# Optimization experiments

Hardware: AMD Instinct MI355X
Metric: run time of the kernel (lower is better)

Reference implementation:

```python
import jax, jax.numpy as jnp
import numpy as np

N, E = 50000, 800000
IN_DIM, HID, HEADS, LAYERS = 128, 128, 4, 2
C = HID // HEADS  # per-head channels
LN_EPS = 1e-5


def _segment_softmax(logits, seg, num_segments):
    # logits: [E, H], seg: [E] target-node ids
    m = jax.ops.segment_max(logits, seg, num_segments=num_segments)  # [N, H]
    ex = jnp.exp(logits - m[seg])
    s = jax.ops.segment_sum(ex, seg, num_segments=num_segments)      # [N, H]
    return ex / s[seg]


def setup_inputs() -> dict:
    key = jax.random.key(0)
    ks = jax.random.split(key, 16)
    x = jax.random.normal(ks[0], (N, IN_DIM), dtype=jnp.float32)
    edge_index = jax.random.randint(ks[1], (2, E), 0, N, dtype=jnp.int64)
    edge_weight = jax.random.normal(ks[2], (E,), dtype=jnp.float32)
    s = 0.05
    # stacked per-layer params (in_ch == hidden for both layers since in_dim == hidden_dim)
    Wq = jax.random.normal(ks[3], (LAYERS, HID, HID), dtype=jnp.float32) * s
    bq = jnp.zeros((LAYERS, HID), dtype=jnp.float32)
    Wk = jax.random.normal(ks[4], (LAYERS, HID, HID), dtype=jnp.float32) * s
    bk = jnp.zeros((LAYERS, HID), dtype=jnp.float32)
    Wv = jax.random.normal(ks[5], (LAYERS, HID, HID), dtype=jnp.float32) * s
    bv = jnp.zeros((LAYERS, HID), dtype=jnp.float32)
    We = jax.random.normal(ks[6], (LAYERS, 1, HID), dtype=jnp.float32) * s  # lin_edge, no bias
    Wskip = jax.random.normal(ks[7], (LAYERS, HID, HID), dtype=jnp.float32) * s
    bskip = jnp.zeros((LAYERS, HID), dtype=jnp.float32)
    ln_g = jnp.ones((LAYERS, HID), dtype=jnp.float32)
    ln_b = jnp.zeros((LAYERS, HID), dtype=jnp.float32)
    return dict(x=x, edge_index=edge_index, edge_weight=edge_weight,
                Wq=Wq, bq=bq, Wk=Wk, bk=bk, Wv=Wv, bv=bv, We=We,
                Wskip=Wskip, bskip=bskip, ln_g=ln_g, ln_b=ln_b)


def reference(x, edge_index, edge_weight, Wq, bq, Wk, bk, Wv, bv, We, Wskip, bskip, ln_g, ln_b):
    # eval mode: dropout (on alpha and on features) is identity
    h = jnp.nan_to_num(x, nan=0.0, posinf=0.0, neginf=0.0)
    edge_attr = jnp.nan_to_num(edge_weight, nan=0.0, posinf=0.0, neginf=0.0)[:, None]  # [E,1]
    src, dst = edge_index[0], edge_index[1]  # PyG: x_j = x[src], softmax/aggregate over dst
    scale = 1.0 / jnp.sqrt(jnp.asarray(C, dtype=h.dtype))
    for l in range(LAYERS):
        h_res = h
        q = (h @ Wq[l] + bq[l]).reshape(N, HEADS, C)
        k = (h @ Wk[l] + bk[l]).reshape(N, HEADS, C)
        v = (h @ Wv[l] + bv[l]).reshape(N, HEADS, C)
        e = (edge_attr @ We[l]).reshape(E, HEADS, C)          # lin_edge (bias=False)
        kj = k[src] + e                                       # [E,H,C]
        logits = jnp.einsum('ehc,ehc->eh', q[dst], kj) * scale
        alpha = _segment_softmax(logits, dst, N)              # [E,H]
        msg = (v[src] + e) * alpha[..., None]                 # [E,H,C]
        out = jax.ops.segment_sum(msg, dst, num_segments=N).reshape(N, HID)
        out = out + h @ Wskip[l] + bskip[l]                   # root_weight skip (beta=False)
        out = jnp.nan_to_num(out, nan=0.0, posinf=0.0, neginf=0.0)
        mu = out.mean(axis=-1, keepdims=True)
        var = ((out - mu) ** 2).mean(axis=-1, keepdims=True)
        out = (out - mu) / jnp.sqrt(var + LN_EPS) * ln_g[l] + ln_b[l]
        out = jax.nn.relu(jnp.nan_to_num(out, nan=0.0, posinf=0.0, neginf=0.0))
        out = jnp.nan_to_num(out, nan=0.0, posinf=0.0, neginf=0.0)
        h = jnp.nan_to_num(out + h_res, nan=0.0, posinf=0.0, neginf=0.0)
    return h
```

## Files before the change

kernel.cpp:

```cpp
#include <hip/hip_runtime.h>
#include <hip/hip_fp16.h>
#include <math.h>

#define NN 50000
#define EE 800000
#define HID 128
#define LAYERS 2
#define LN_EPS 1e-5f
#define SCALE 0.17677669529663687f

typedef _Float16 f16x8 __attribute__((ext_vector_type(8)));
typedef float f32x4 __attribute__((ext_vector_type(4)));

__device__ __forceinline__ float sanitize(float f) {
    return (f == f && fabsf(f) != INFINITY) ? f : 0.0f;
}


__global__ void zero_deg_kernel(int* __restrict__ deg) {
    int i = blockIdx.x * blockDim.x + threadIdx.x;
    if (i < NN) deg[i] = 0;
}

__global__ void hist_kernel(const int* __restrict__ eidx, int* __restrict__ deg) {
    int e = blockIdx.x * blockDim.x + threadIdx.x;
    if (e < EE) atomicAdd(&deg[eidx[EE + e]], 1);
}

__global__ __launch_bounds__(1024) void scan_kernel(const int* __restrict__ deg,
                                                    int* __restrict__ row_start,
                                                    int* __restrict__ cursor) {
    __shared__ int wsum[16];
    __shared__ int carry_s;
    int tid = threadIdx.x;
    int lane = tid & 63;
    int wid = tid >> 6;
    if (tid == 0) carry_s = 0;
    __syncthreads();
    for (int base = 0; base < NN; base += 1024) {
        int i = base + tid;
        int val = (i < NN) ? deg[i] : 0;
        int sc = val;
        #pragma unroll
        for (int off = 1; off < 64; off <<= 1) {
            int t = __shfl_up(sc, off, 64);
            if (lane >= off) sc += t;
        }
        if (lane == 63) wsum[wid] = sc;
        __syncthreads();
        if (wid == 0) {
            int s = (lane < 16) ? wsum[lane] : 0;
            #pragma unroll
            for (int off = 1; off < 16; off <<= 1) {
                int t = __shfl_up(s, off, 64);
                if (lane >= off) s += t;
            }
            if (lane < 16) wsum[lane] = s;
        }
        __syncthreads();
        int waveoff = (wid > 0) ? wsum[wid - 1] : 0;
        int excl = carry_s + waveoff + sc - val;
        if (i < NN) {
            row_start[i] = excl;
            cursor[i] = excl;
        }
        __syncthreads();
        if (tid == 0) carry_s += wsum[15];
        __syncthreads();
    }
    if (tid == 0) row_start[NN] = carry_s;
}

__global__ void scatter_kernel(const int* __restrict__ eidx,
                               const float* __restrict__ ew,
                               int* __restrict__ cursor,
                               long long* __restrict__ csr_pk) {
    int e = blockIdx.x * blockDim.x + threadIdx.x;
    if (e < EE) {
        int dst = eidx[EE + e];
        int src = eidx[e];
        int pos = atomicAdd(&cursor[dst], 1);
        unsigned wb = __float_as_uint(sanitize(ew[e]));
        csr_pk[pos] = ((long long)wb << 32) | (unsigned)src;
    }
}


__global__ void sanitize_kernel(const float* __restrict__ x, float* __restrict__ h0,
                                __half* __restrict__ hh) {
    int i = blockIdx.x * blockDim.x + threadIdx.x;
    if (i < NN * HID / 4) {
        float4 f = ((const float4*)x)[i];
        f.x = sanitize(f.x); f.y = sanitize(f.y); f.z = sanitize(f.z); f.w = sanitize(f.w);
        ((float4*)h0)[i] = f;
        __half2* hp = (__half2*)(hh + (size_t)i * 4);
        hp[0] = __floats2half2_rn(f.x, f.y);
        hp[1] = __floats2half2_rn(f.z, f.w);
    }
}


__global__ void wtcvt_kernel(const float* __restrict__ Wq, const float* __restrict__ Wk,
                             const float* __restrict__ Wv, __half* __restrict__ WT) {
    int idx = blockIdx.x * blockDim.x + threadIdx.x;
    if (idx >= LAYERS * 3 * HID * HID) return;
    int k = idx & 127;
    int c = (idx >> 7) & 127;
    int lm = idx >> 14;
    int m = lm % 3;
    int l = lm / 3;
    const float* W = (m == 0) ? Wq : (m == 1) ? Wk : Wv;
    WT[idx] = __float2half(W[l * HID * HID + k * HID + c]);
}


__global__ __launch_bounds__(256) void mfma_qkv_kernel(
    const __half* __restrict__ hh, const __half* __restrict__ WT,
    const float* __restrict__ bq, const float* __restrict__ bk, const float* __restrict__ bv,
    __half* __restrict__ qh, __half* __restrict__ kv)
{
    int wid = threadIdx.x >> 6;
    int lane = threadIdx.x & 63;
    int row0 = blockIdx.x * 64 + wid * 16;
    int arow = row0 + (lane & 15);
    if (arow >= NN) arow = NN - 1;
    int ksub = (lane >> 4) * 8;

    const _Float16* hp = (const _Float16*)(hh + (size_t)arow * HID + ksub);
    f16x8 a0 = *(const f16x8*)(hp + 0);
    f16x8 a1 = *(const f16x8*)(hp + 32);
    f16x8 a2 = *(const f16x8*)(hp + 64);
    f16x8 a3 = *(const f16x8*)(hp + 96);

    #pragma unroll
    for (int m = 0; m < 3; ++m) {
        const _Float16* Wm = (const _Float16*)(WT + m * HID * HID);
        const float* bias = (m == 0) ? bq : (m == 1) ? bk : bv;
        #pragma unroll
        for (int t = 0; t < 8; ++t) {
            int col = t * 16 + (lane & 15);
            const _Float16* wc = Wm + (size_t)col * HID + ksub;
            f32x4 acc = {0.f, 0.f, 0.f, 0.f};
            acc = __builtin_amdgcn_mfma_f32_16x16x32_f16(a0, *(const f16x8*)(wc + 0),  acc, 0, 0, 0);
            acc = __builtin_amdgcn_mfma_f32_16x16x32_f16(a1, *(const f16x8*)(wc + 32), acc, 0, 0, 0);
            acc = __builtin_amdgcn_mfma_f32_16x16x32_f16(a2, *(const f16x8*)(wc + 64), acc, 0, 0, 0);
            acc = __builtin_amdgcn_mfma_f32_16x16x32_f16(a3, *(const f16x8*)(wc + 96), acc, 0, 0, 0);
            float bcol = bias[col];
            #pragma unroll
            for (int r = 0; r < 4; ++r) {
                int row = row0 + (lane >> 4) * 4 + r;
                if (row < NN) {
                    __half val = __float2half(acc[r] + bcol);
                    if (m == 0)      qh[(size_t)row * HID + col] = val;
                    else if (m == 1) kv[(size_t)row * 256 + col] = val;
                    else             kv[(size_t)row * 256 + 128 + col] = val;
                }
            }
        }
    }
}


#define GR 64
#define GK 32

__global__ __launch_bounds__(256) void gemm_skip_kernel(
    const float* __restrict__ hin, const float* __restrict__ W,
    const float* __restrict__ b, float* __restrict__ o)
{
    __shared__ float sh[GR][GK];
    __shared__ float sw[GK][HID];

    const int tid = threadIdx.x;
    const int cg = tid & 31;
    const int rg = tid >> 5;
    const int row0 = blockIdx.x * GR;

    float4 acc[8];
    #pragma unroll
    for (int r = 0; r < 8; ++r) acc[r] = make_float4(0.f, 0.f, 0.f, 0.f);

    for (int kc = 0; kc < HID; kc += GK) {
        __syncthreads();
        #pragma unroll
        for (int p = 0; p < 2; ++p) {
            int idx = p * 256 + tid;
            int r = idx >> 3;
            int c4 = idx & 7;
            int grow = row0 + r;
            float4 hv = make_float4(0.f, 0.f, 0.f, 0.f);
            if (grow < NN) hv = *(const float4*)(hin + (size_t)grow * HID + kc + c4 * 4);
            *(float4*)(&sh[r][c4 * 4]) = hv;
        }
        #pragma unroll
        for (int p = 0; p < 4; ++p) {
            int idx = p * 256 + tid;
            ((float4*)sw)[idx] = ((const float4*)(W + (size_t)kc * HID))[idx];
        }
        __syncthreads();

        #pragma unroll
        for (int k4 = 0; k4 < GK; k4 += 4) {
            float4 b0 = *(float4*)(&sw[k4 + 0][cg * 4]);
            float4 b1 = *(float4*)(&sw[k4 + 1][cg * 4]);
            float4 b2 = *(float4*)(&sw[k4 + 2][cg * 4]);
            float4 b3 = *(float4*)(&sw[k4 + 3][cg * 4]);
            #pragma unroll
            for (int rr = 0; rr < 8; ++rr) {
                float4 a = *(float4*)(&sh[rg * 8 + rr][k4]);
                float4 t = acc[rr];
                t.x = fmaf(a.x, b0.x, fmaf(a.y, b1.x, fmaf(a.z, b2.x, fmaf(a.w, b3.x, t.x))));
                t.y = fmaf(a.x, b0.y, fmaf(a.y, b1.y, fmaf(a.z, b2.y, fmaf(a.w, b3.y, t.y))));
                t.z = fmaf(a.x, b0.z, fmaf(a.y, b1.z, fmaf(a.z, b2.z, fmaf(a.w, b3.z, t.z))));
                t.w = fmaf(a.x, b0.w, fmaf(a.y, b1.w, fmaf(a.z, b2.w, fmaf(a.w, b3.w, t.w))));
                acc[rr] = t;
            }
        }
    }

    float4 bias = *(const float4*)(b + cg * 4);
    #pragma unroll
    for (int rr = 0; rr < 8; ++rr) {
        int grow = row0 + rg * 8 + rr;
        if (grow < NN) {
            float4 t = acc[rr];
            t.x += bias.x; t.y += bias.y; t.z += bias.z; t.w += bias.w;
            *(float4*)(o + (size_t)grow * HID + cg * 4) = t;
        }
    }
}


__device__ __forceinline__ float red16(float x) {
    #pragma unroll
    for (int off = 8; off >= 1; off >>= 1) x += __shfl_xor(x, off, 16);
    return x;
}

__device__ __forceinline__ float red64(float x) {
    #pragma unroll
    for (int off = 32; off >= 1; off >>= 1) x += __shfl_xor(x, off, 64);
    return x;
}

struct OS { float m, s, tw, ax, ay; };

__device__ __forceinline__ void os_init(OS& o) {
    o.m = -INFINITY; o.s = 0.f; o.tw = 0.f; o.ax = 0.f; o.ay = 0.f;
}

__device__ __forceinline__ void os_upd(OS& o, float l, float w, float vx, float vy) {
    float mn = fmaxf(o.m, l);
    float cr = __expf(o.m - mn);
    float p  = __expf(l - mn);
    o.s  = fmaf(o.s,  cr, p);
    o.tw = fmaf(o.tw, cr, p * w);
    o.ax = fmaf(o.ax, cr, p * vx);
    o.ay = fmaf(o.ay, cr, p * vy);
    o.m = mn;
}

__device__ __forceinline__ OS os_mrg(OS a, OS b) {
    float mn = fmaxf(a.m, b.m);
    if (mn == -INFINITY) return a;
    float ca = __expf(a.m - mn);
    float cb = __expf(b.m - mn);
    OS r;
    r.m = mn;
    r.s  = a.s  * ca + b.s  * cb;
    r.tw = a.tw * ca + b.tw * cb;
    r.ax = a.ax * ca + b.ax * cb;
    r.ay = a.ay * ca + b.ay * cb;
    return r;
}

__device__ __forceinline__ void edge_step(const long long* __restrict__ csr_pk, int i,
                                          const __half* __restrict__ kv, int lane,
                                          float qx, float qy, float qwe, OS& st) {
    long long p = csr_pk[i];
    int src = (int)(p & 0xffffffffLL);
    float w = __uint_as_float((unsigned)((unsigned long long)p >> 32));
    const __half* kvp = kv + (size_t)src * 256;
    float2 k2 = __half22float2(*(const __half2*)(kvp + 2 * lane));
    float2 v2 = __half22float2(*(const __half2*)(kvp + 128 + 2 * lane));
    float d = red16(fmaf(k2.x, qx, k2.y * qy));
    float l = fmaf(w, qwe, d) * SCALE;
    os_upd(st, l, w, v2.x, v2.y);
}

__global__ __launch_bounds__(256) void agg_kernel(
    const __half* __restrict__ qh, const __half* __restrict__ kv,
    const float* __restrict__ skp, const float* __restrict__ hres,
    const float* __restrict__ We,
    const float* __restrict__ ln_g, const float* __restrict__ ln_b,
    const int* __restrict__ row_start, const long long* __restrict__ csr_pk,
    float* __restrict__ hout, __half* __restrict__ hh_out)
{
    int node = blockIdx.x * 4 + (threadIdx.x >> 6);
    if (node >= NN) return;
    int lane = threadIdx.x & 63;
    int c0 = lane * 2;

    float2 q2 = __half22float2(*(const __half2*)(qh + (size_t)node * HID + c0));
    float2 we2 = *(const float2*)(We + c0);
    float qwe = red16(fmaf(q2.x, we2.x, q2.y * we2.y));

    int rs = row_start[node];
    int re = row_start[node + 1];

    OS st0, st1, st2, st3;
    os_init(st0); os_init(st1); os_init(st2); os_init(st3);

    int i = rs;
    for (; i + 4 <= re; i += 4) {
        edge_step(csr_pk, i + 0, kv, lane, q2.x, q2.y, qwe, st0);
        edge_step(csr_pk, i + 1, kv, lane, q2.x, q2.y, qwe, st1);
        edge_step(csr_pk, i + 2, kv, lane, q2.x, q2.y, qwe, st2);
        edge_step(csr_pk, i + 3, kv, lane, q2.x, q2.y, qwe, st3);
    }
    for (; i < re; ++i) edge_step(csr_pk, i, kv, lane, q2.x, q2.y, qwe, st0);

    OS st = os_mrg(os_mrg(st0, st1), os_mrg(st2, st3));

    float ox = 0.f, oy = 0.f;
    if (re > rs) {
        float inv = 1.f / st.s;
        ox = fmaf(st.tw, we2.x, st.ax) * inv;
        oy = fmaf(st.tw, we2.y, st.ay) * inv;
    }

    float2 sk = *(const float2*)(skp + (size_t)node * HID + c0);
    ox = sanitize(ox + sk.x);
    oy = sanitize(oy + sk.y);

    float mu = red64(ox + oy) * (1.f / 128.f);
    float dx = ox - mu, dy = oy - mu;
    float var = red64(fmaf(dx, dx, dy * dy)) * (1.f / 128.f);
    float rstd = rsqrtf(var + LN_EPS);

    float2 g = *(const float2*)(ln_g + c0);
    float2 bb = *(const float2*)(ln_b + c0);
    float rx = fmaxf(fmaf(dx * rstd, g.x, bb.x), 0.f);
    float ry = fmaxf(fmaf(dy * rstd, g.y, bb.y), 0.f);

    float2 hr = *(const float2*)(hres + (size_t)node * HID + c0);
    float outx = sanitize(rx + hr.x);
    float outy = sanitize(ry + hr.y);
    *(float2*)(hout + (size_t)node * HID + c0) = make_float2(outx, outy);
    *(__half2*)(hh_out + (size_t)node * HID + c0) = __floats2half2_rn(outx, outy);
}


extern "C" void kernel_launch(void* const* d_in, const int* in_sizes, int n_in,
                              void* d_out, int out_size, void* d_ws, size_t ws_size,
                              hipStream_t stream) {
    const float* x      = (const float*)d_in[0];
    const int*   ei     = (const int*)d_in[1];
    const float* ew     = (const float*)d_in[2];
    const float* Wq     = (const float*)d_in[3];
    const float* bq     = (const float*)d_in[4];
    const float* Wk     = (const float*)d_in[5];
    const float* bk     = (const float*)d_in[6];
    const float* Wv     = (const float*)d_in[7];
    const float* bv     = (const float*)d_in[8];
    const float* We     = (const float*)d_in[9];
    const float* Wsk    = (const float*)d_in[10];
    const float* bsk    = (const float*)d_in[11];
    const float* ln_g   = (const float*)d_in[12];
    const float* ln_b   = (const float*)d_in[13];

    const size_t NH = (size_t)NN * HID;
    float* h0 = (float*)d_ws;
    float* h1 = h0 + NH;
    float* sk = h1 + NH;
    __half* hh = (__half*)(sk + NH);
    __half* qh = hh + NH;
    __half* kv = qh + NH;
    __half* WT = kv + 2 * NH;
    int* deg       = (int*)(WT + LAYERS * 3 * HID * HID);
    int* row_start = deg + NN;
    int* cursor    = row_start + NN + 2;
    long long* csr_pk = (long long*)(cursor + NN);

    zero_deg_kernel<<<(NN + 255) / 256, 256, 0, stream>>>(deg);
    hist_kernel<<<(EE + 255) / 256, 256, 0, stream>>>(ei, deg);
    scan_kernel<<<1, 1024, 0, stream>>>(deg, row_start, cursor);
    scatter_kernel<<<(EE + 255) / 256, 256, 0, stream>>>(ei, ew, cursor, csr_pk);

    sanitize_kernel<<<(NN * HID / 4 + 255) / 256, 256, 0, stream>>>(x, h0, hh);
    wtcvt_kernel<<<(LAYERS * 3 * HID * HID + 255) / 256, 256, 0, stream>>>(Wq, Wk, Wv, WT);

    const int WELEM = HID * HID;
    const int MROWS = (NN + 63) / 64;

    for (int l = 0; l < LAYERS; ++l) {
        const float* hin = (l == 0) ? h0 : h1;
        float* hout = (l == 0) ? h1 : (float*)d_out;
        mfma_qkv_kernel<<<MROWS, 256, 0, stream>>>(
            hh, WT + (size_t)l * 3 * WELEM,
            bq + l * HID, bk + l * HID, bv + l * HID,
            qh, kv);
        gemm_skip_kernel<<<MROWS, 256, 0, stream>>>(hin, Wsk + l * WELEM, bsk + l * HID, sk);
        agg_kernel<<<(NN + 3) / 4, 256, 0, stream>>>(
            qh, kv, sk, hin,
            We + l * HID, ln_g + l * HID, ln_b + l * HID,
            row_start, csr_pk, hout, hh);
    }
}
```

Baseline: 562.2 us.

## Fuse skip GEMM into MFMA QKV kernel, narrow agg to 16 lanes/node, parallel scan

Three separate changes. The skip projection moves off its fp32 SIMT GEMM kernel and becomes a fourth fp16 MFMA output in the QKV kernel, which drops one kernel launch and one full read of the fp32 activations. The aggregation kernel now gives each node 16 lanes that each own 8 channels, using vectorized 16-byte gathers and fdot2, instead of 64 lanes with 2 channels each. This cuts shuffle reductions and packs 16 nodes per block. The single-block degree scan becomes a three-kernel multi-block scan. The skip GEMM now runs on fp16 inputs and weights, which lowers its precision.

```diff
diff --git a/kernel.cpp b/kernel.cpp
--- a/kernel.cpp
+++ b/kernel.cpp
@@ -8,8 +8,10 @@
 #define LAYERS 2
 #define LN_EPS 1e-5f
 #define SCALE 0.17677669529663687f
+#define NB 49
 
 typedef _Float16 f16x8 __attribute__((ext_vector_type(8)));
+typedef _Float16 h2 __attribute__((ext_vector_type(2)));
 typedef float f32x4 __attribute__((ext_vector_type(4)));
 
 __device__ __forceinline__ float sanitize(float f) {
@@ -27,48 +29,73 @@
     if (e < EE) atomicAdd(&deg[eidx[EE + e]], 1);
 }
 
-__global__ __launch_bounds__(1024) void scan_kernel(const int* __restrict__ deg,
-                                                    int* __restrict__ row_start,
-                                                    int* __restrict__ cursor) {
+
+__global__ __launch_bounds__(1024) void deg_bsum_kernel(const int* __restrict__ deg,
+                                                        int* __restrict__ bsum) {
+    __shared__ int red[16];
+    int tid = threadIdx.x;
+    int i = blockIdx.x * 1024 + tid;
+    int v = (i < NN) ? deg[i] : 0;
+    #pragma unroll
+    for (int off = 32; off >= 1; off >>= 1) v += __shfl_xor(v, off, 64);
+    if ((tid & 63) == 0) red[tid >> 6] = v;
+    __syncthreads();
+    if (tid == 0) {
+        int s = 0;
+        #pragma unroll
+        for (int w = 0; w < 16; ++w) s += red[w];
+        bsum[blockIdx.x] = s;
+    }
+}
+
+__global__ void bsum_scan_kernel(const int* __restrict__ bsum, int* __restrict__ boff,
+                                 int* __restrict__ row_start) {
+    int lane = threadIdx.x;
+    int v = (lane < NB) ? bsum[lane] : 0;
+    int sc = v;
+    #pragma unroll
+    for (int off = 1; off < 64; off <<= 1) {
+        int t = __shfl_up(sc, off, 64);
+        if (lane >= off) sc += t;
+    }
+    if (lane < NB) boff[lane] = sc - v;
+    if (lane == 63) row_start[NN] = sc;
+}
+
+__global__ __launch_bounds__(1024) void deg_scan_kernel(const int* __restrict__ deg,
+                                                        const int* __restrict__ boff,
+                                                        int* __restrict__ row_start,
+                                                        int* __restrict__ cursor) {
     __shared__ int wsum[16];
-    __shared__ int carry_s;
     int tid = threadIdx.x;
     int lane = tid & 63;
     int wid = tid >> 6;
-    if (tid == 0) carry_s = 0;
+    int i = blockIdx.x * 1024 + tid;
+    int val = (i < NN) ? deg[i] : 0;
+    int sc = val;
+    #pragma unroll
+    for (int off = 1; off < 64; off <<= 1) {
+        int t = __shfl_up(sc, off, 64);
+        if (lane >= off) sc += t;
+    }
+    if (lane == 63) wsum[wid] = sc;
     __syncthreads();
-    for (int base = 0; base < NN; base += 1024) {
-        int i = base + tid;
-        int val = (i < NN) ? deg[i] : 0;
-        int sc = val;
+    if (wid == 0) {
+        int s = (lane < 16) ? wsum[lane] : 0;
         #pragma unroll
-        for (int off = 1; off < 64; off <<= 1) {
-            int t = __shfl_up(sc, off, 64);
-            if (lane >= off) sc += t;
+        for (int off = 1; off < 16; off <<= 1) {
+            int t = __shfl_up(s, off, 64);
+            if (lane >= off) s += t;
         }
-        if (lane == 63) wsum[wid] = sc;
-        __syncthreads();
-        if (wid == 0) {
-            int s = (lane < 16) ? wsum[lane] : 0;
-            #pragma unroll
-            for (int off = 1; off < 16; off <<= 1) {
-                int t = __shfl_up(s, off, 64);
-                if (lane >= off) s += t;
-            }
-            if (lane < 16) wsum[lane] = s;
-        }
-        __syncthreads();
-        int waveoff = (wid > 0) ? wsum[wid - 1] : 0;
-        int excl = carry_s + waveoff + sc - val;
-        if (i < NN) {
-            row_start[i] = excl;
-            cursor[i] = excl;
-        }
-        __syncthreads();
-        if (tid == 0) carry_s += wsum[15];
-        __syncthreads();
-    }
-    if (tid == 0) row_start[NN] = carry_s;
+        if (lane < 16) wsum[lane] = s;
+    }
+    __syncthreads();
+    int waveoff = (wid > 0) ? wsum[wid - 1] : 0;
+    int excl = boff[blockIdx.x] + waveoff + sc - val;
+    if (i < NN) {
+        row_start[i] = excl;
+        cursor[i] = excl;
+    }
 }
 
 __global__ void scatter_kernel(const int* __restrict__ eidx,
@@ -101,23 +128,24 @@
 
 
 __global__ void wtcvt_kernel(const float* __restrict__ Wq, const float* __restrict__ Wk,
-                             const float* __restrict__ Wv, __half* __restrict__ WT) {
+                             const float* __restrict__ Wv, const float* __restrict__ Wsk,
+                             __half* __restrict__ WT) {
     int idx = blockIdx.x * blockDim.x + threadIdx.x;
-    if (idx >= LAYERS * 3 * HID * HID) return;
+    if (idx >= LAYERS * 4 * HID * HID) return;
     int k = idx & 127;
     int c = (idx >> 7) & 127;
-    int lm = idx >> 14;
-    int m = lm % 3;
-    int l = lm / 3;
-    const float* W = (m == 0) ? Wq : (m == 1) ? Wk : Wv;
+    int m = (idx >> 14) & 3;
+    int l = idx >> 16;
+    const float* W = (m == 0) ? Wq : (m == 1) ? Wk : (m == 2) ? Wv : Wsk;
     WT[idx] = __float2half(W[l * HID * HID + k * HID + c]);
 }
 
 
-__global__ __launch_bounds__(256) void mfma_qkv_kernel(
+__global__ __launch_bounds__(256) void mfma_qkvs_kernel(
     const __half* __restrict__ hh, const __half* __restrict__ WT,
-    const float* __restrict__ bq, const float* __restrict__ bk, const float* __restrict__ bv,
-    __half* __restrict__ qh, __half* __restrict__ kv)
+    const float* __restrict__ bq, const float* __restrict__ bk,
+    const float* __restrict__ bv, const float* __restrict__ bsk,
+    __half* __restrict__ qh, __half* __restrict__ kv, float* __restrict__ skf)
 {
     int wid = threadIdx.x >> 6;
     int lane = threadIdx.x & 63;
@@ -133,9 +161,9 @@
     f16x8 a3 = *(const f16x8*)(hp + 96);
 
     #pragma unroll
-    for (int m = 0; m < 3; ++m) {
+    for (int m = 0; m < 4; ++m) {
         const _Float16* Wm = (const _Float16*)(WT + m * HID * HID);
-        const float* bias = (m == 0) ? bq : (m == 1) ? bk : bv;
+        const float* bias = (m == 0) ? bq : (m == 1) ? bk : (m == 2) ? bv : bsk;
         #pragma unroll
         for (int t = 0; t < 8; ++t) {
             int col = t * 16 + (lane & 15);
@@ -150,10 +178,11 @@
             for (int r = 0; r < 4; ++r) {
                 int row = row0 + (lane >> 4) * 4 + r;
                 if (row < NN) {
-                    __half val = __float2half(acc[r] + bcol);
-                    if (m == 0)      qh[(size_t)row * HID + col] = val;
-                    else if (m == 1) kv[(size_t)row * 256 + col] = val;
-                    else             kv[(size_t)row * 256 + 128 + col] = val;
+                    float val = acc[r] + bcol;
+                    if (m == 0)      qh[(size_t)row * HID + col] = __float2half(val);
+                    else if (m == 1) kv[(size_t)row * 256 + col] = __float2half(val);
+                    else if (m == 2) kv[(size_t)row * 256 + 128 + col] = __float2half(val);
+                    else             skf[(size_t)row * HID + col] = val;
                 }
             }
         }
@@ -161,131 +190,51 @@
 }
 
 
-#define GR 64
-#define GK 32
-
-__global__ __launch_bounds__(256) void gemm_skip_kernel(
-    const float* __restrict__ hin, const float* __restrict__ W,
-    const float* __restrict__ b, float* __restrict__ o)
-{
-    __shared__ float sh[GR][GK];
-    __shared__ float sw[GK][HID];
-
-    const int tid = threadIdx.x;
-    const int cg = tid & 31;
-    const int rg = tid >> 5;
-    const int row0 = blockIdx.x * GR;
-
-    float4 acc[8];
-    #pragma unroll
-    for (int r = 0; r < 8; ++r) acc[r] = make_float4(0.f, 0.f, 0.f, 0.f);
-
-    for (int kc = 0; kc < HID; kc += GK) {
-        __syncthreads();
-        #pragma unroll
-        for (int p = 0; p < 2; ++p) {
-            int idx = p * 256 + tid;
-            int r = idx >> 3;
-            int c4 = idx & 7;
-            int grow = row0 + r;
-            float4 hv = make_float4(0.f, 0.f, 0.f, 0.f);
-            if (grow < NN) hv = *(const float4*)(hin + (size_t)grow * HID + kc + c4 * 4);
-            *(float4*)(&sh[r][c4 * 4]) = hv;
-        }
-        #pragma unroll
-        for (int p = 0; p < 4; ++p) {
-            int idx = p * 256 + tid;
-            ((float4*)sw)[idx] = ((const float4*)(W + (size_t)kc * HID))[idx];
-        }
-        __syncthreads();
-
-        #pragma unroll
-        for (int k4 = 0; k4 < GK; k4 += 4) {
-            float4 b0 = *(float4*)(&sw[k4 + 0][cg * 4]);
-            float4 b1 = *(float4*)(&sw[k4 + 1][cg * 4]);
-            float4 b2 = *(float4*)(&sw[k4 + 2][cg * 4]);
-            float4 b3 = *(float4*)(&sw[k4 + 3][cg * 4]);
-            #pragma unroll
-            for (int rr = 0; rr < 8; ++rr) {
-                float4 a = *(float4*)(&sh[rg * 8 + rr][k4]);
-                float4 t = acc[rr];
-                t.x = fmaf(a.x, b0.x, fmaf(a.y, b1.x, fmaf(a.z, b2.x, fmaf(a.w, b3.x, t.x))));
-                t.y = fmaf(a.x, b0.y, fmaf(a.y, b1.y, fmaf(a.z, b2.y, fmaf(a.w, b3.y, t.y))));
-                t.z = fmaf(a.x, b0.z, fmaf(a.y, b1.z, fmaf(a.z, b2.z, fmaf(a.w, b3.z, t.z))));
-                t.w = fmaf(a.x, b0.w, fmaf(a.y, b1.w, fmaf(a.z, b2.w, fmaf(a.w, b3.w, t.w))));
-                acc[rr] = t;
-            }
-        }
-    }
-
-    float4 bias = *(const float4*)(b + cg * 4);
-    #pragma unroll
-    for (int rr = 0; rr < 8; ++rr) {
-        int grow = row0 + rg * 8 + rr;
-        if (grow < NN) {
-            float4 t = acc[rr];
-            t.x += bias.x; t.y += bias.y; t.z += bias.z; t.w += bias.w;
-            *(float4*)(o + (size_t)grow * HID + cg * 4) = t;
-        }
-    }
-}
-
-
-__device__ __forceinline__ float red16(float x) {
-    #pragma unroll
-    for (int off = 8; off >= 1; off >>= 1) x += __shfl_xor(x, off, 16);
-    return x;
-}
-
-__device__ __forceinline__ float red64(float x) {
-    #pragma unroll
-    for (int off = 32; off >= 1; off >>= 1) x += __shfl_xor(x, off, 64);
-    return x;
-}
-
-struct OS { float m, s, tw, ax, ay; };
-
-__device__ __forceinline__ void os_init(OS& o) {
-    o.m = -INFINITY; o.s = 0.f; o.tw = 0.f; o.ax = 0.f; o.ay = 0.f;
-}
-
-__device__ __forceinline__ void os_upd(OS& o, float l, float w, float vx, float vy) {
-    float mn = fmaxf(o.m, l);
-    float cr = __expf(o.m - mn);
-    float p  = __expf(l - mn);
-    o.s  = fmaf(o.s,  cr, p);
-    o.tw = fmaf(o.tw, cr, p * w);
-    o.ax = fmaf(o.ax, cr, p * vx);
-    o.ay = fmaf(o.ay, cr, p * vy);
-    o.m = mn;
-}
-
-__device__ __forceinline__ OS os_mrg(OS a, OS b) {
+struct OS8 { float m, s, tw; float a[8]; };
+
+__device__ __forceinline__ void os8_init(OS8& o) {
+    o.m = -INFINITY; o.s = 0.f; o.tw = 0.f;
+    #pragma unroll
+    for (int j = 0; j < 8; ++j) o.a[j] = 0.f;
+}
+
+__device__ __forceinline__ OS8 os8_mrg(OS8 a, OS8 b) {
     float mn = fmaxf(a.m, b.m);
     if (mn == -INFINITY) return a;
     float ca = __expf(a.m - mn);
     float cb = __expf(b.m - mn);
-    OS r;
+    OS8 r;
     r.m = mn;
     r.s  = a.s  * ca + b.s  * cb;
     r.tw = a.tw * ca + b.tw * cb;
-    r.ax = a.ax * ca + b.ax * cb;
-    r.ay = a.ay * ca + b.ay * cb;
+    #pragma unroll
+    for (int j = 0; j < 8; ++j) r.a[j] = a.a[j] * ca + b.a[j] * cb;
     return r;
 }
 
-__device__ __forceinline__ void edge_step(const long long* __restrict__ csr_pk, int i,
-                                          const __half* __restrict__ kv, int lane,
-                                          float qx, float qy, float qwe, OS& st) {
-    long long p = csr_pk[i];
+__device__ __forceinline__ void edge_step(long long p, const __half* __restrict__ kv, int c0,
+                                          h2 q01, h2 q23, h2 q45, h2 q67, float qwe, OS8& st) {
     int src = (int)(p & 0xffffffffLL);
     float w = __uint_as_float((unsigned)((unsigned long long)p >> 32));
-    const __half* kvp = kv + (size_t)src * 256;
-    float2 k2 = __half22float2(*(const __half2*)(kvp + 2 * lane));
-    float2 v2 = __half22float2(*(const __half2*)(kvp + 128 + 2 * lane));
-    float d = red16(fmaf(k2.x, qx, k2.y * qy));
+    const _Float16* kvp = (const _Float16*)(kv + (size_t)src * 256);
+    f16x8 k8 = *(const f16x8*)(kvp + c0);
+    f16x8 v8 = *(const f16x8*)(kvp + 128 + c0);
+    h2 k01 = {k8[0], k8[1]}, k23 = {k8[2], k8[3]}, k45 = {k8[4], k8[5]}, k67 = {k8[6], k8[7]};
+    float d = __builtin_amdgcn_fdot2(k01, q01, 0.f, false);
+    d = __builtin_amdgcn_fdot2(k23, q23, d, false);
+    d = __builtin_amdgcn_fdot2(k45, q45, d, false);
+    d = __builtin_amdgcn_fdot2(k67, q67, d, false);
+    d += __shfl_xor(d, 1, 64);
+    d += __shfl_xor(d, 2, 64);
     float l = fmaf(w, qwe, d) * SCALE;
-    os_upd(st, l, w, v2.x, v2.y);
+    float mn = fmaxf(st.m, l);
+    float cr = __expf(st.m - mn);
+    float pp = __expf(l - mn);
+    st.s  = fmaf(st.s,  cr, pp);
+    st.tw = fmaf(st.tw, cr, pp * w);
+    #pragma unroll
+    for (int j = 0; j < 8; ++j) st.a[j] = fmaf(st.a[j], cr, pp * (float)v8[j]);
+    st.m = mn;
 }
 
 __global__ __launch_bounds__(256) void agg_kernel(
@@ -296,58 +245,100 @@
     const int* __restrict__ row_start, const long long* __restrict__ csr_pk,
     float* __restrict__ hout, __half* __restrict__ hh_out)
 {
-    int node = blockIdx.x * 4 + (threadIdx.x >> 6);
-    if (node >= NN) return;
-    int lane = threadIdx.x & 63;
-    int c0 = lane * 2;
-
-    float2 q2 = __half22float2(*(const __half2*)(qh + (size_t)node * HID + c0));
-    float2 we2 = *(const float2*)(We + c0);
-    float qwe = red16(fmaf(q2.x, we2.x, q2.y * we2.y));
+    int node = blockIdx.x * 16 + (threadIdx.x >> 4);
+    int sl = threadIdx.x & 15;
+    int c0 = sl * 8;
+
+    f16x8 q8 = *(const f16x8*)((const _Float16*)qh + (size_t)node * HID + c0);
+    h2 q01 = {q8[0], q8[1]}, q23 = {q8[2], q8[3]}, q45 = {q8[4], q8[5]}, q67 = {q8[6], q8[7]};
+
+    float4 weA = *(const float4*)(We + c0);
+    float4 weB = *(const float4*)(We + c0 + 4);
+    float qwe = (float)q8[0] * weA.x + (float)q8[1] * weA.y + (float)q8[2] * weA.z + (float)q8[3] * weA.w
+              + (float)q8[4] * weB.x + (float)q8[5] * weB.y + (float)q8[6] * weB.z + (float)q8[7] * weB.w;
+    qwe += __shfl_xor(qwe, 1, 64);
+    qwe += __shfl_xor(qwe, 2, 64);
 
     int rs = row_start[node];
     int re = row_start[node + 1];
 
-    OS st0, st1, st2, st3;
-    os_init(st0); os_init(st1); os_init(st2); os_init(st3);
+    OS8 st0, st1, st2, st3;
+    os8_init(st0); os8_init(st1); os8_init(st2); os8_init(st3);
 
     int i = rs;
     for (; i + 4 <= re; i += 4) {
-        edge_step(csr_pk, i + 0, kv, lane, q2.x, q2.y, qwe, st0);
-        edge_step(csr_pk, i + 1, kv, lane, q2.x, q2.y, qwe, st1);
-        edge_step(csr_pk, i + 2, kv, lane, q2.x, q2.y, qwe, st2);
-        edge_step(csr_pk, i + 3, kv, lane, q2.x, q2.y, qwe, st3);
-    }
-    for (; i < re; ++i) edge_step(csr_pk, i, kv, lane, q2.x, q2.y, qwe, st0);
-
-    OS st = os_mrg(os_mrg(st0, st1), os_mrg(st2, st3));
-
-    float ox = 0.f, oy = 0.f;
-    if (re > rs) {
-        float inv = 1.f / st.s;
-        ox = fmaf(st.tw, we2.x, st.ax) * inv;
-        oy = fmaf(st.tw, we2.y, st.ay) * inv;
-    }
-
-    float2 sk = *(const float2*)(skp + (size_t)node * HID + c0);
-    ox = sanitize(ox + sk.x);
-    oy = sanitize(oy + sk.y);
-
-    float mu = red64(ox + oy) * (1.f / 128.f);
-    float dx = ox - mu, dy = oy - mu;
-    float var = red64(fmaf(dx, dx, dy * dy)) * (1.f / 128.f);
+        long long p0 = csr_pk[i + 0];
+        long long p1 = csr_pk[i + 1];
+        long long p2 = csr_pk[i + 2];
+        long long p3 = csr_pk[i + 3];
+        edge_step(p0, kv, c0, q01, q23, q45, q67, qwe, st0);
+        edge_step(p1, kv, c0, q01, q23, q45, q67, qwe, st1);
+        edge_step(p2, kv, c0, q01, q23, q45, q67, qwe, st2);
+        edge_step(p3, kv, c0, q01, q23, q45, q67, qwe, st3);
+    }
+    for (; i < re; ++i) edge_step(csr_pk[i], kv, c0, q01, q23, q45, q67, qwe, st0);
+
+    OS8 st = os8_mrg(os8_mrg(st0, st1), os8_mrg(st2, st3));
+
+    float inv = (re > rs) ? 1.f / st.s : 0.f;
+    float wef[8] = {weA.x, weA.y, weA.z, weA.w, weB.x, weB.y, weB.z, weB.w};
+
+    float4 skA = *(const float4*)(skp + (size_t)node * HID + c0);
+    float4 skB = *(const float4*)(skp + (size_t)node * HID + c0 + 4);
+    float skv[8] = {skA.x, skA.y, skA.z, skA.w, skB.x, skB.y, skB.z, skB.w};
+
+    float ox[8];
+    float sum8 = 0.f;
+    #pragma unroll
+    for (int j = 0; j < 8; ++j) {
+        float o = fmaf(st.tw, wef[j], st.a[j]) * inv;
+        o = sanitize(o + skv[j]);
+        ox[j] = o;
+        sum8 += o;
+    }
+
+    float mu = sum8;
+    mu += __shfl_xor(mu, 1, 64); mu += __shfl_xor(mu, 2, 64);
+    mu += __shfl_xor(mu, 4, 64); mu += __shfl_xor(mu, 8, 64);
+    mu *= (1.f / 128.f);
+
+    float var8 = 0.f;
+    #pragma unroll
+    for (int j = 0; j < 8; ++j) {
+        float dx = ox[j] - mu;
+        var8 = fmaf(dx, dx, var8);
+    }
+    float var = var8;
+    var += __shfl_xor(var, 1, 64); var += __shfl_xor(var, 2, 64);
+    var += __shfl_xor(var, 4, 64); var += __shfl_xor(var, 8, 64);
+    var *= (1.f / 128.f);
     float rstd = rsqrtf(var + LN_EPS);
 
-    float2 g = *(const float2*)(ln_g + c0);
-    float2 bb = *(const float2*)(ln_b + c0);
-    float rx = fmaxf(fmaf(dx * rstd, g.x, bb.x), 0.f);
-    float ry = fmaxf(fmaf(dy * rstd, g.y, bb.y), 0.f);
-
-    float2 hr = *(const float2*)(hres + (size_t)node * HID + c0);
-    float outx = sanitize(rx + hr.x);
-    float outy = sanitize(ry + hr.y);
-    *(float2*)(hout + (size_t)node * HID + c0) = make_float2(outx, outy);
-    *(__half2*)(hh_out + (size_t)node * HID + c0) = __floats2half2_rn(outx, outy);
+    float4 gA = *(const float4*)(ln_g + c0);
+    float4 gB = *(const float4*)(ln_g + c0 + 4);
+    float4 bA = *(const float4*)(ln_b + c0);
+    float4 bB = *(const float4*)(ln_b + c0 + 4);
+    float gv[8] = {gA.x, gA.y, gA.z, gA.w, gB.x, gB.y, gB.z, gB.w};
+    float bv_[8] = {bA.x, bA.y, bA.z, bA.w, bB.x, bB.y, bB.z, bB.w};
+
+    float4 hrA = *(const float4*)(hres + (size_t)node * HID + c0);
+    float4 hrB = *(const float4*)(hres + (size_t)node * HID + c0 + 4);
+    float hr[8] = {hrA.x, hrA.y, hrA.z, hrA.w, hrB.x, hrB.y, hrB.z, hrB.w};
+
+    float outv[8];
+    _Float16 outh[8];
+    #pragma unroll
+    for (int j = 0; j < 8; ++j) {
+        float rx = fmaxf(fmaf((ox[j] - mu) * rstd, gv[j], bv_[j]), 0.f);
+        float o = sanitize(rx + hr[j]);
+        outv[j] = o;
+        outh[j] = (_Float16)o;
+    }
+    float* op = hout + (size_t)node * HID + c0;
+    *(float4*)(op)     = make_float4(outv[0], outv[1], outv[2], outv[3]);
+    *(float4*)(op + 4) = make_float4(outv[4], outv[5], outv[6], outv[7]);
+    *(f16x8*)((_Float16*)hh_out + (size_t)node * HID + c0) =
+        *(f16x8*)outh;
 }
 
 
@@ -370,25 +361,29 @@
     const float* ln_b   = (const float*)d_in[13];
 
     const size_t NH = (size_t)NN * HID;
-    float* h0 = (float*)d_ws;
-    float* h1 = h0 + NH;
-    float* sk = h1 + NH;
-    __half* hh = (__half*)(sk + NH);
+    float* h0  = (float*)d_ws;
+    float* h1  = h0 + NH;
+    float* skf = h1 + NH;
+    __half* hh = (__half*)(skf + NH);
     __half* qh = hh + NH;
     __half* kv = qh + NH;
     __half* WT = kv + 2 * NH;
-    int* deg       = (int*)(WT + LAYERS * 3 * HID * HID);
+    int* deg       = (int*)(WT + LAYERS * 4 * HID * HID);
     int* row_start = deg + NN;
     int* cursor    = row_start + NN + 2;
-    long long* csr_pk = (long long*)(cursor + NN);
+    int* bsum      = cursor + NN;
+    int* boff      = bsum + 64;
+    long long* csr_pk = (long long*)(boff + 64);
 
     zero_deg_kernel<<<(NN + 255) / 256, 256, 0, stream>>>(deg);
     hist_kernel<<<(EE + 255) / 256, 256, 0, stream>>>(ei, deg);
-    scan_kernel<<<1, 1024, 0, stream>>>(deg, row_start, cursor);
+    deg_bsum_kernel<<<NB, 1024, 0, stream>>>(deg, bsum);
+    bsum_scan_kernel<<<1, 64, 0, stream>>>(bsum, boff, row_start);
+    deg_scan_kernel<<<NB, 1024, 0, stream>>>(deg, boff, row_start, cursor);
     scatter_kernel<<<(EE + 255) / 256, 256, 0, stream>>>(ei, ew, cursor, csr_pk);
 
     sanitize_kernel<<<(NN * HID / 4 + 255) / 256, 256, 0, stream>>>(x, h0, hh);
-    wtcvt_kernel<<<(LAYERS * 3 * HID * HID + 255) / 256, 256, 0, stream>>>(Wq, Wk, Wv, WT);
+    wtcvt_kernel<<<(LAYERS * 4 * HID * HID + 255) / 256, 256, 0, stream>>>(Wq, Wk, Wv, Wsk, WT);
 
     const int WELEM = HID * HID;
     const int MROWS = (NN + 63) / 64;
@@ -396,13 +391,12 @@
     for (int l = 0; l < LAYERS; ++l) {
         const float* hin = (l == 0) ? h0 : h1;
         float* hout = (l == 0) ? h1 : (float*)d_out;
-        mfma_qkv_kernel<<<MROWS, 256, 0, stream>>>(
-            hh, WT + (size_t)l * 3 * WELEM,
-            bq + l * HID, bk + l * HID, bv + l * HID,
-            qh, kv);
-        gemm_skip_kernel<<<MROWS, 256, 0, stream>>>(hin, Wsk + l * WELEM, bsk + l * HID, sk);
-        agg_kernel<<<(NN + 3) / 4, 256, 0, stream>>>(
-            qh, kv, sk, hin,
+        mfma_qkvs_kernel<<<MROWS, 256, 0, stream>>>(
+            hh, WT + (size_t)l * 4 * WELEM,
+            bq + l * HID, bk + l * HID, bv + l * HID, bsk + l * HID,
+            qh, kv, skf);
+        agg_kernel<<<NN / 16, 256, 0, stream>>>(
+            qh, kv, skf, hin,
             We + l * HID, ln_g + l * HID, ln_b + l * HID,
             row_start, csr_pk, hout, hh);
     }
```

Measured after the change: 472.8 us. 1.19x faster.
